# Optimization experiments

Measured on AMD Instinct MI355X. Metric: run time of the kernel, lower is better.

## Reference

```python
import jax, jax.numpy as jnp
import numpy as np
from jax import lax

B_, L, DM = 2, 2048, 1024
DI, N, K, R = 2048, 16, 4, 64  # d_inner, d_state, d_conv, dt_rank
EPS = 1e-5


def setup_inputs() -> dict:
    key = jax.random.key(0)
    ks = jax.random.split(key, 12)
    w = lambda k, s: (jax.random.normal(k, s, dtype=jnp.float32) * 0.02)
    inp = {
        "x": jax.random.normal(ks[0], (B_, L, DM), dtype=jnp.float32),
        "hormone_vectors": jax.random.normal(ks[1], (B_, 64), dtype=jnp.float32),
        "norm_w": jnp.ones((DM,), dtype=jnp.float32),
        "in_proj_w": w(ks[2], (DM, 2 * DI)),
        "conv_w": w(ks[3], (DI, K)),
        "conv_b": jnp.zeros((DI,), dtype=jnp.float32),
        "x_proj_w": w(ks[4], (DI, R + 2 * N)),
        "dt_proj_w": w(ks[5], (R, DI)),
        "dt_proj_b": jax.random.uniform(ks[6], (DI,), dtype=jnp.float32, minval=-4.0, maxval=-2.0),
        "A_log": jnp.log(jnp.broadcast_to(jnp.arange(1, N + 1, dtype=jnp.float32), (DI, N))),
        "D": jnp.ones((DI,), dtype=jnp.float32),
        "out_proj_w": w(ks[7], (DI, DM)),
    }
    return inp


def _rmsnorm(x, w, eps=EPS):
    var = jnp.mean(x * x, axis=-1, keepdims=True)
    return x * lax.rsqrt(var + eps) * w


def _causal_depthwise_conv(u, conv_w, conv_b):
    # u: [B,L,DI] -> causal depthwise conv along L with kernel K
    lhs = jnp.transpose(u, (0, 2, 1))  # [B,DI,L]
    lhs = jnp.pad(lhs, ((0, 0), (0, 0), (K - 1, 0)))
    rhs = conv_w[:, None, :]  # [DI,1,K]
    out = lax.conv_general_dilated(
        lhs, rhs, window_strides=(1,), padding="VALID",
        dimension_numbers=("NCH", "OIH", "NCH"), feature_group_count=DI)
    return jnp.transpose(out, (0, 2, 1)) + conv_b  # [B,L,DI]


def _mamba_mixer(h, in_proj_w, conv_w, conv_b, x_proj_w, dt_proj_w, dt_proj_b,
                 A_log, D, out_proj_w):
    xz = h @ in_proj_w                       # [B,L,2*DI]
    u, z = jnp.split(xz, 2, axis=-1)         # each [B,L,DI]
    u = jax.nn.silu(_causal_depthwise_conv(u, conv_w, conv_b))

    xdbl = u @ x_proj_w                      # [B,L,R+2N]
    dt_r = xdbl[..., :R]
    Bm = xdbl[..., R:R + N]                  # [B,L,N]
    Cm = xdbl[..., R + N:]                   # [B,L,N]
    dt = jax.nn.softplus(dt_r @ dt_proj_w + dt_proj_b)  # [B,L,DI]
    A = -jnp.exp(A_log)                      # [DI,N]

    def step(hst, inp):
        dt_t, B_t, C_t, u_t = inp            # [B,DI],[B,N],[B,N],[B,DI]
        dA = jnp.exp(dt_t[..., None] * A)                         # [B,DI,N]
        dBu = dt_t[..., None] * B_t[:, None, :] * u_t[..., None]  # [B,DI,N]
        hst = dA * hst + dBu
        y = jnp.einsum("bdn,bn->bd", hst, C_t)
        return hst, y

    xs = (jnp.swapaxes(dt, 0, 1), jnp.swapaxes(Bm, 0, 1),
          jnp.swapaxes(Cm, 0, 1), jnp.swapaxes(u, 0, 1))
    h0 = jnp.zeros((u.shape[0], DI, N), dtype=u.dtype)
    _, ys = lax.scan(step, h0, xs)
    y = jnp.swapaxes(ys, 0, 1) + u * D       # [B,L,DI]
    y = y * jax.nn.silu(z)
    return y @ out_proj_w                    # [B,L,DM]


def reference(x, hormone_vectors, norm_w, in_proj_w, conv_w, conv_b, x_proj_w,
              dt_proj_w, dt_proj_b, A_log, D, out_proj_w):
    del hormone_vectors  # unused, matching original module
    h = _rmsnorm(x, norm_w)
    return x + _mamba_mixer(h, in_proj_w, conv_w, conv_b, x_proj_w,
                            dt_proj_w, dt_proj_b, A_log, D, out_proj_w)
```

## Files before the change

kernel.cpp:

```cpp
#include <hip/hip_runtime.h>
#include <stddef.h>

#define B_SZ 2
#define L_SZ 2048
#define DM_SZ 1024
#define DI_SZ 2048
#define N_SZ 16
#define K_SZ 4
#define R_SZ 64
#define ROWS (B_SZ * L_SZ)
#define CH 32
#define NCH (L_SZ / CH)
#define PS_SLICE (B_SZ * DI_SZ * N_SZ)

typedef unsigned short u16;
typedef unsigned int u32;
typedef short bf16x8 __attribute__((ext_vector_type(8)));
typedef float f32x4 __attribute__((ext_vector_type(4)));

__device__ __forceinline__ u16 f2bf(float f) {
    union { float f; u32 i; } v; v.f = f;
    u32 x = v.i;
    return (u16)((x + 0x7FFFu + ((x >> 16) & 1u)) >> 16);
}
__device__ __forceinline__ float bf2f(u16 u) {
    union { u32 i; float f; } v; v.i = ((u32)u) << 16; return v.f;
}

__device__ __forceinline__ void gload_lds16(const void* g, void* l) {
    __builtin_amdgcn_global_load_lds((const __attribute__((address_space(1))) u32*)g,
                                     (__attribute__((address_space(3))) u32*)l, 16, 0, 0);
}

__global__ __launch_bounds__(256) void rmsnorm_kernel(const float* __restrict__ x,
                                                      const float* __restrict__ w,
                                                      u16* __restrict__ h) {
    const int row = blockIdx.x;
    const float* xr = x + (size_t)row * DM_SZ;
    const int t4 = threadIdx.x * 4;
    float4 xv = *(const float4*)(xr + t4);
    float ss = xv.x * xv.x + xv.y * xv.y + xv.z * xv.z + xv.w * xv.w;
    #pragma unroll
    for (int off = 32; off; off >>= 1) ss += __shfl_down(ss, off);
    __shared__ float red[4];
    if ((threadIdx.x & 63) == 0) red[threadIdx.x >> 6] = ss;
    __syncthreads();
    float tot = red[0] + red[1] + red[2] + red[3];
    float rs = rsqrtf(tot * (1.0f / DM_SZ) + 1e-5f);
    float4 wv = *(const float4*)(w + t4);
    ushort4 o;
    o.x = f2bf(xv.x * rs * wv.x);
    o.y = f2bf(xv.y * rs * wv.y);
    o.z = f2bf(xv.z * rs * wv.z);
    o.w = f2bf(xv.w * rs * wv.w);
    *(ushort4*)(h + (size_t)row * DM_SZ + t4) = o;
}

__global__ __launch_bounds__(256) void transpose_bf16_kernel(const float* __restrict__ W,
                                                             u16* __restrict__ Wt,
                                                             int K, int N) {
    __shared__ float t[32][33];
    const int n0 = blockIdx.x * 32, k0 = blockIdx.y * 32;
    const int tx = threadIdx.x & 31, ty = threadIdx.x >> 5;
    #pragma unroll
    for (int p = 0; p < 4; ++p)
        t[ty + p * 8][tx] = W[(size_t)(k0 + ty + p * 8) * N + n0 + tx];
    __syncthreads();
    #pragma unroll
    for (int p = 0; p < 4; ++p)
        Wt[(size_t)(n0 + ty + p * 8) * K + k0 + tx] = f2bf(t[tx][ty + p * 8]);
}

template <bool HAS_RESID>
__global__ __launch_bounds__(256, 2) void mfma_gemm_bt(const u16* __restrict__ A,
                                                       const u16* __restrict__ Bt,
                                                       float* __restrict__ C,
                                                       const float* __restrict__ resid,
                                                       int M, int N, int Kd) {
    __shared__ __align__(16) u16 As[128 * 32];
    __shared__ __align__(16) u16 Bs[128 * 32];
    const int tid = threadIdx.x;
    const int lane = tid & 63;
    const int w = tid >> 6;
    const int wm = w >> 1, wn = w & 1;
    const int bm = blockIdx.y * 128, bn = blockIdx.x * 128;

    const int r0 = (w * 2 + 0) * 16 + (lane >> 2);
    const int r1 = (w * 2 + 1) * 16 + (lane >> 2);
    const int kc = (lane & 3) * 8;
    const u16* Aq0 = A + (size_t)(bm + r0) * Kd + kc;
    const u16* Aq1 = A + (size_t)(bm + r1) * Kd + kc;
    const u16* Bq0 = Bt + (size_t)(bn + r0) * Kd + kc;
    const u16* Bq1 = Bt + (size_t)(bn + r1) * Kd + kc;
    u16* lA0 = As + (w * 2 + 0) * 512;
    u16* lA1 = As + (w * 2 + 1) * 512;
    u16* lB0 = Bs + (w * 2 + 0) * 512;
    u16* lB1 = Bs + (w * 2 + 1) * 512;

    f32x4 acc[4][4] = {};
    const int fm = (lane & 15);
    const int q8 = (lane >> 4) * 8;

    for (int k0 = 0; k0 < Kd; k0 += 32) {
        gload_lds16(Aq0 + k0, lA0);
        gload_lds16(Aq1 + k0, lA1);
        gload_lds16(Bq0 + k0, lB0);
        gload_lds16(Bq1 + k0, lB1);
        __syncthreads();
        bf16x8 af[4], bf[4];
        #pragma unroll
        for (int i = 0; i < 4; ++i)
            af[i] = *(const bf16x8*)&As[(wm * 64 + i * 16 + fm) * 32 + q8];
        #pragma unroll
        for (int j = 0; j < 4; ++j)
            bf[j] = *(const bf16x8*)&Bs[(wn * 64 + j * 16 + fm) * 32 + q8];
        #pragma unroll
        for (int i = 0; i < 4; ++i)
            #pragma unroll
            for (int j = 0; j < 4; ++j)
                acc[i][j] = __builtin_amdgcn_mfma_f32_16x16x32_bf16(af[i], bf[j], acc[i][j], 0, 0, 0);
        __syncthreads();
    }

    const int crow0 = bm + wm * 64 + (lane >> 4) * 4;
    const int ccol0 = bn + wn * 64 + (lane & 15);
    #pragma unroll
    for (int i = 0; i < 4; ++i) {
        #pragma unroll
        for (int r = 0; r < 4; ++r) {
            const int row = crow0 + i * 16 + r;
            #pragma unroll
            for (int j = 0; j < 4; ++j) {
                const int col = ccol0 + j * 16;
                float v = acc[i][j][r];
                if (HAS_RESID) v += resid[(size_t)row * N + col];
                C[(size_t)row * N + col] = v;
            }
        }
    }
}

__global__ __launch_bounds__(256) void conv_silu_kernel(const float* __restrict__ xz,
                                                        const float* __restrict__ cw,
                                                        const float* __restrict__ cb,
                                                        u16* __restrict__ u) {
    const int idx = blockIdx.x * 256 + threadIdx.x;
    const int d = idx & (DI_SZ - 1);
    const int r = idx >> 11;
    const int t = r & (L_SZ - 1);
    float4 w4 = *(const float4*)(cw + (d << 2));
    const float w[4] = {w4.x, w4.y, w4.z, w4.w};
    float acc = cb[d];
    const float* base = xz + (size_t)r * (2 * DI_SZ) + d;
    #pragma unroll
    for (int k = 0; k < 4; ++k) {
        int tt = t - 3 + k;
        if (tt >= 0) acc += base[(ptrdiff_t)(k - 3) * (2 * DI_SZ)] * w[k];
    }
    u[idx] = f2bf(acc / (1.0f + __expf(-acc)));
}

__global__ __launch_bounds__(256) void xproj_mfma(const u16* __restrict__ ubf,
                                                  const u16* __restrict__ Wt,
                                                  float* __restrict__ xdbl) {
    const int lane = threadIdx.x & 63;
    const int w = threadIdx.x >> 6;
    const int m0 = blockIdx.x * 64 + w * 16;
    const int k0 = blockIdx.y * 256;
    const int fr = lane & 15;
    const int q8 = (lane >> 4) * 8;
    const u16* Arow = ubf + (size_t)(m0 + fr) * DI_SZ + k0 + q8;
    const u16* Brow = Wt + (size_t)fr * DI_SZ + k0 + q8;
    f32x4 acc[6] = {};
    #pragma unroll 2
    for (int kk = 0; kk < 256; kk += 32) {
        bf16x8 a = *(const bf16x8*)(Arow + kk);
        #pragma unroll
        for (int j = 0; j < 6; ++j) {
            bf16x8 b = *(const bf16x8*)(Brow + (size_t)(j * 16) * DI_SZ + kk);
            acc[j] = __builtin_amdgcn_mfma_f32_16x16x32_bf16(a, b, acc[j], 0, 0, 0);
        }
    }
    const int row0 = m0 + (lane >> 4) * 4;
    const int col = lane & 15;
    #pragma unroll
    for (int j = 0; j < 6; ++j)
        #pragma unroll
        for (int r = 0; r < 4; ++r)
            atomicAdd(&xdbl[(size_t)(row0 + r) * 96 + j * 16 + col], acc[j][r]);
}

__global__ __launch_bounds__(256) void dtslice_bf16_kernel(const float* __restrict__ xdbl,
                                                           u16* __restrict__ out) {
    const int idx = blockIdx.x * 256 + threadIdx.x;
    const int r = idx >> 6, k = idx & 63;
    out[idx] = f2bf(xdbl[(size_t)r * 96 + k]);
}

__global__ __launch_bounds__(256, 2) void dtproj_mfma(const u16* __restrict__ Axd,
                                                      const u16* __restrict__ Wt,
                                                      const float* __restrict__ bias,
                                                      u16* __restrict__ dt) {
    __shared__ __align__(16) u16 As[128 * 64];
    __shared__ __align__(16) u16 Bs[128 * 64];
    const int tid = threadIdx.x;
    const int lane = tid & 63;
    const int w = tid >> 6;
    const int wm = w >> 1, wn = w & 1;
    const int bm = blockIdx.y * 128, bn = blockIdx.x * 128;

    #pragma unroll
    for (int q = 0; q < 4; ++q) {
        const int rr = (w * 4 + q) * 8 + (lane >> 3);
        const int kc = (lane & 7) * 8;
        gload_lds16(Axd + (size_t)(bm + rr) * 64 + kc, As + (w * 4 + q) * 512);
        gload_lds16(Wt  + (size_t)(bn + rr) * 64 + kc, Bs + (w * 4 + q) * 512);
    }
    __syncthreads();

    const int fm = lane & 15;
    const int q8 = (lane >> 4) * 8;
    f32x4 acc[4][4] = {};
    #pragma unroll
    for (int k0 = 0; k0 < 64; k0 += 32) {
        bf16x8 af[4], bf[4];
        #pragma unroll
        for (int i = 0; i < 4; ++i)
            af[i] = *(const bf16x8*)&As[(wm * 64 + i * 16 + fm) * 64 + k0 + q8];
        #pragma unroll
        for (int j = 0; j < 4; ++j)
            bf[j] = *(const bf16x8*)&Bs[(wn * 64 + j * 16 + fm) * 64 + k0 + q8];
        #pragma unroll
        for (int i = 0; i < 4; ++i)
            #pragma unroll
            for (int j = 0; j < 4; ++j)
                acc[i][j] = __builtin_amdgcn_mfma_f32_16x16x32_bf16(af[i], bf[j], acc[i][j], 0, 0, 0);
    }

    const int crow0 = bm + wm * 64 + (lane >> 4) * 4;
    const int ccol0 = bn + wn * 64 + (lane & 15);
    #pragma unroll
    for (int j = 0; j < 4; ++j) {
        const int col = ccol0 + j * 16;
        const float b = bias[col];
        #pragma unroll
        for (int i = 0; i < 4; ++i) {
            #pragma unroll
            for (int r = 0; r < 4; ++r) {
                const int row = crow0 + i * 16 + r;
                float v = acc[i][j][r] + b;
                float sp = (v > 20.0f) ? v : log1pf(__expf(v));
                dt[(size_t)row * DI_SZ + col] = f2bf(sp);
            }
        }
    }
}

__global__ __launch_bounds__(64) void scan_pass1(const u16* __restrict__ dt,
                                                 const u16* __restrict__ u,
                                                 const float* __restrict__ xdbl,
                                                 const float* __restrict__ A_log,
                                                 float* __restrict__ P,
                                                 float* __restrict__ S) {
    const int c     = blockIdx.x & (NCH - 1);
    const int dtile = (blockIdx.x >> 6) & 31;
    const int b     = blockIdx.x >> 11;
    const int d     = dtile * 64 + threadIdx.x;
    float A[N_SZ];
    #pragma unroll
    for (int n = 0; n < N_SZ; ++n) A[n] = -expf(A_log[d * N_SZ + n]);
    __shared__ __align__(16) float bs[CH][16];
    const size_t rbase = (size_t)b * L_SZ + c * CH;
    for (int idx = threadIdx.x; idx < CH * 16; idx += 64) {
        int tt = idx >> 4, j = idx & 15;
        bs[tt][j] = xdbl[(rbase + tt) * 96 + 64 + j];
    }
    __syncthreads();
    float h[N_SZ] = {};
    float p[N_SZ];
    #pragma unroll
    for (int n = 0; n < N_SZ; ++n) p[n] = 1.0f;
    float dtv = bf2f(dt[rbase * DI_SZ + d]);
    float uv  = bf2f(u[rbase * DI_SZ + d]);
    for (int ti = 0; ti < CH; ++ti) {
        float dtn = 0.0f, un = 0.0f;
        if (ti + 1 < CH) {
            dtn = bf2f(dt[(rbase + ti + 1) * DI_SZ + d]);
            un  = bf2f(u[(rbase + ti + 1) * DI_SZ + d]);
        }
        const float dtu = dtv * uv;
        float bv[N_SZ];
        #pragma unroll
        for (int q = 0; q < 4; ++q) *(float4*)&bv[q * 4] = *(const float4*)&bs[ti][q * 4];
        #pragma unroll
        for (int n = 0; n < N_SZ; ++n) {
            float dA = __expf(dtv * A[n]);
            p[n] *= dA;
            h[n] = dA * h[n] + dtu * bv[n];
        }
        dtv = dtn; uv = un;
    }
    const size_t base = (size_t)c * PS_SLICE + ((size_t)b * DI_SZ + d) * N_SZ;
    #pragma unroll
    for (int q = 0; q < 4; ++q) {
        *(float4*)&P[base + q * 4] = make_float4(p[q*4], p[q*4+1], p[q*4+2], p[q*4+3]);
        *(float4*)&S[base + q * 4] = make_float4(h[q*4], h[q*4+1], h[q*4+2], h[q*4+3]);
    }
}

__global__ __launch_bounds__(256) void scan_pass2(float* __restrict__ P,
                                                  float* __restrict__ S) {
    const int i = blockIdx.x * 256 + threadIdx.x;
    float h = 0.0f;
    for (int c = 0; c < NCH; ++c) {
        const size_t idx = (size_t)c * PS_SLICE + i;
        const float p = P[idx];
        const float s = S[idx];
        S[idx] = h;
        h = p * h + s;
    }
}

__global__ __launch_bounds__(64) void scan_pass3(const u16* __restrict__ dt,
                                                 const u16* __restrict__ u,
                                                 const float* __restrict__ xz,
                                                 const float* __restrict__ xdbl,
                                                 const float* __restrict__ A_log,
                                                 const float* __restrict__ Dw,
                                                 const float* __restrict__ H0,
                                                 u16* __restrict__ y) {
    const int c     = blockIdx.x & (NCH - 1);
    const int dtile = (blockIdx.x >> 6) & 31;
    const int b     = blockIdx.x >> 11;
    const int d     = dtile * 64 + threadIdx.x;
    float A[N_SZ];
    #pragma unroll
    for (int n = 0; n < N_SZ; ++n) A[n] = -expf(A_log[d * N_SZ + n]);
    const float Dd = Dw[d];
    __shared__ __align__(16) float bc[CH][32];
    const size_t rbase = (size_t)b * L_SZ + c * CH;
    for (int idx = threadIdx.x; idx < CH * 32; idx += 64) {
        int tt = idx >> 5, j = idx & 31;
        bc[tt][j] = xdbl[(rbase + tt) * 96 + 64 + j];
    }
    __syncthreads();
    float h[N_SZ];
    const size_t hbase = (size_t)c * PS_SLICE + ((size_t)b * DI_SZ + d) * N_SZ;
    #pragma unroll
    for (int q = 0; q < 4; ++q) *(float4*)&h[q * 4] = *(const float4*)&H0[hbase + q * 4];
    float dtv = bf2f(dt[rbase * DI_SZ + d]);
    float uv  = bf2f(u[rbase * DI_SZ + d]);
    float zv  = xz[rbase * (2 * DI_SZ) + DI_SZ + d];
    for (int ti = 0; ti < CH; ++ti) {
        float dtn = 0.0f, un = 0.0f, zn = 0.0f;
        if (ti + 1 < CH) {
            const size_t rn = rbase + ti + 1;
            dtn = bf2f(dt[rn * DI_SZ + d]);
            un  = bf2f(u[rn * DI_SZ + d]);
            zn  = xz[rn * (2 * DI_SZ) + DI_SZ + d];
        }
        const float dtu = dtv * uv;
        float bv[32];
        #pragma unroll
        for (int q = 0; q < 8; ++q) *(float4*)&bv[q * 4] = *(const float4*)&bc[ti][q * 4];
        float yv = 0.0f;
        #pragma unroll
        for (int n = 0; n < N_SZ; ++n) {
            float dA = __expf(dtv * A[n]);
            h[n] = dA * h[n] + dtu * bv[n];
            yv += h[n] * bv[16 + n];
        }
        const float sz = zv / (1.0f + __expf(-zv));
        y[(rbase + ti) * DI_SZ + d] = f2bf((yv + uv * Dd) * sz);
        dtv = dtn; uv = un; zv = zn;
    }
}

extern "C" void kernel_launch(void* const* d_in, const int* in_sizes, int n_in,
                              void* d_out, int out_size, void* d_ws, size_t ws_size,
                              hipStream_t stream) {
    const float* x         = (const float*)d_in[0];
    const float* norm_w    = (const float*)d_in[2];
    const float* in_proj_w = (const float*)d_in[3];
    const float* conv_w    = (const float*)d_in[4];
    const float* conv_b    = (const float*)d_in[5];
    const float* x_proj_w  = (const float*)d_in[6];
    const float* dt_proj_w = (const float*)d_in[7];
    const float* dt_proj_b = (const float*)d_in[8];
    const float* A_log     = (const float*)d_in[9];
    const float* Dw        = (const float*)d_in[10];
    const float* out_proj_w= (const float*)d_in[11];
    float* out = (float*)d_out;

    char* ws = (char*)d_ws;
    size_t off = 0;
    u16* y      = (u16*)(ws + off);    off += (size_t)ROWS * DI_SZ * 2;
    u16* h      = y;
    float* xz   = (float*)(ws + off);  off += (size_t)ROWS * 2 * DI_SZ * 4;
    u16* u      = (u16*)(ws + off);    off += (size_t)ROWS * DI_SZ * 2;
    float* xdbl = (float*)(ws + off);  off += (size_t)ROWS * 96 * 4;
    u16* dt     = (u16*)(ws + off);    off += (size_t)ROWS * DI_SZ * 2;
    float* P    = (float*)(ws + off);  off += (size_t)NCH * PS_SLICE * 4;
    float* S    = (float*)(ws + off);  off += (size_t)NCH * PS_SLICE * 4;
    u16* ipw_t  = (u16*)(ws + off);    off += (size_t)(2 * DI_SZ) * DM_SZ * 2;
    u16* opw_t  = (u16*)(ws + off);    off += (size_t)DM_SZ * DI_SZ * 2;
    u16* xpw_t  = (u16*)(ws + off);    off += (size_t)96 * DI_SZ * 2;
    u16* dtw_t  = (u16*)(ws + off);    off += (size_t)DI_SZ * R_SZ * 2;
    u16* xdbl_bf= (u16*)(ws + off);    off += (size_t)ROWS * R_SZ * 2;
    (void)ws_size; (void)out_size; (void)n_in; (void)in_sizes;

    rmsnorm_kernel<<<ROWS, 256, 0, stream>>>(x, norm_w, h);
    transpose_bf16_kernel<<<dim3(2 * DI_SZ / 32, DM_SZ / 32), 256, 0, stream>>>(
        in_proj_w, ipw_t, DM_SZ, 2 * DI_SZ);
    transpose_bf16_kernel<<<dim3(DM_SZ / 32, DI_SZ / 32), 256, 0, stream>>>(
        out_proj_w, opw_t, DI_SZ, DM_SZ);
    transpose_bf16_kernel<<<dim3(96 / 32, DI_SZ / 32), 256, 0, stream>>>(
        x_proj_w, xpw_t, DI_SZ, 96);
    transpose_bf16_kernel<<<dim3(DI_SZ / 32, R_SZ / 32), 256, 0, stream>>>(
        dt_proj_w, dtw_t, R_SZ, DI_SZ);
    mfma_gemm_bt<false><<<dim3(2 * DI_SZ / 128, ROWS / 128), 256, 0, stream>>>(
        h, ipw_t, xz, nullptr, ROWS, 2 * DI_SZ, DM_SZ);
    conv_silu_kernel<<<(ROWS * DI_SZ) / 256, 256, 0, stream>>>(xz, conv_w, conv_b, u);
    hipMemsetAsync(xdbl, 0, (size_t)ROWS * 96 * 4, stream);
    xproj_mfma<<<dim3(ROWS / 64, 8), 256, 0, stream>>>(u, xpw_t, xdbl);
    dtslice_bf16_kernel<<<(ROWS * R_SZ) / 256, 256, 0, stream>>>(xdbl, xdbl_bf);
    dtproj_mfma<<<dim3(DI_SZ / 128, ROWS / 128), 256, 0, stream>>>(
        xdbl_bf, dtw_t, dt_proj_b, dt);
    scan_pass1<<<B_SZ * 32 * NCH, 64, 0, stream>>>(dt, u, xdbl, A_log, P, S);
    scan_pass2<<<PS_SLICE / 256, 256, 0, stream>>>(P, S);
    scan_pass3<<<B_SZ * 32 * NCH, 64, 0, stream>>>(dt, u, xz, xdbl, A_log, Dw, S, y);
    mfma_gemm_bt<true><<<dim3(DM_SZ / 128, ROWS / 128), 256, 0, stream>>>(
        y, opw_t, out, x, ROWS, DM_SZ, DI_SZ);
}
```

Baseline: 375.1 us.

## Store xz in bf16, merge weight transposes, retile out-proj, widen scan chunks

Several changes at once. The in-projection output xz is now stored as bf16 instead of fp32, which halves its write and read traffic in the conv and scan stages. The four weight-transpose launches are merged into one kernel, and the conv/silu kernel is vectorised to four channels per thread. The out-projection GEMM uses 128x64 tiles so more blocks fill the CUs, and the scan chunk length doubles from 32 to 64, giving fewer chunks and a smaller prefix pass. The cost is lower precision for the gate z and the conv input, and less parallelism in the scan.

```diff
diff --git a/kernel.cpp b/kernel.cpp
--- a/kernel.cpp
+++ b/kernel.cpp
@@ -9,7 +9,7 @@
 #define K_SZ 4
 #define R_SZ 64
 #define ROWS (B_SZ * L_SZ)
-#define CH 32
+#define CH 64
 #define NCH (L_SZ / CH)
 #define PS_SLICE (B_SZ * DI_SZ * N_SZ)
 
@@ -56,11 +56,11 @@
     *(ushort4*)(h + (size_t)row * DM_SZ + t4) = o;
 }
 
-__global__ __launch_bounds__(256) void transpose_bf16_kernel(const float* __restrict__ W,
-                                                             u16* __restrict__ Wt,
-                                                             int K, int N) {
+__device__ __forceinline__ void transpose_tile(const float* __restrict__ W,
+                                               u16* __restrict__ Wt,
+                                               int K, int N, int bx, int by) {
     __shared__ float t[32][33];
-    const int n0 = blockIdx.x * 32, k0 = blockIdx.y * 32;
+    const int n0 = bx * 32, k0 = by * 32;
     const int tx = threadIdx.x & 31, ty = threadIdx.x >> 5;
     #pragma unroll
     for (int p = 0; p < 4; ++p)
@@ -71,11 +71,28 @@
         Wt[(size_t)(n0 + ty + p * 8) * K + k0 + tx] = f2bf(t[tx][ty + p * 8]);
 }
 
-template <bool HAS_RESID>
-__global__ __launch_bounds__(256, 2) void mfma_gemm_bt(const u16* __restrict__ A,
+__global__ __launch_bounds__(256) void transpose_all(const float* __restrict__ ipw, u16* __restrict__ ipw_t,
+                                                     const float* __restrict__ opw, u16* __restrict__ opw_t,
+                                                     const float* __restrict__ xpw, u16* __restrict__ xpw_t,
+                                                     const float* __restrict__ dtw, u16* __restrict__ dtw_t) {
+    int b = blockIdx.x;
+    if (b < 4096) {
+        transpose_tile(ipw, ipw_t, DM_SZ, 2 * DI_SZ, b & 127, b >> 7);
+    } else if (b < 6144) {
+        b -= 4096;
+        transpose_tile(opw, opw_t, DI_SZ, DM_SZ, b & 31, b >> 5);
+    } else if (b < 6336) {
+        b -= 6144;
+        transpose_tile(xpw, xpw_t, DI_SZ, 96, b % 3, b / 3);
+    } else {
+        b -= 6336;
+        transpose_tile(dtw, dtw_t, R_SZ, DI_SZ, b & 63, b >> 6);
+    }
+}
+
+__global__ __launch_bounds__(256, 2) void mfma_gemm_xz(const u16* __restrict__ A,
                                                        const u16* __restrict__ Bt,
-                                                       float* __restrict__ C,
-                                                       const float* __restrict__ resid,
+                                                       u16* __restrict__ C,
                                                        int M, int N, int Kd) {
     __shared__ __align__(16) u16 As[128 * 32];
     __shared__ __align__(16) u16 Bs[128 * 32];
@@ -125,39 +142,111 @@
     const int crow0 = bm + wm * 64 + (lane >> 4) * 4;
     const int ccol0 = bn + wn * 64 + (lane & 15);
     #pragma unroll
-    for (int i = 0; i < 4; ++i) {
+    for (int i = 0; i < 4; ++i)
         #pragma unroll
         for (int r = 0; r < 4; ++r) {
             const int row = crow0 + i * 16 + r;
             #pragma unroll
-            for (int j = 0; j < 4; ++j) {
+            for (int j = 0; j < 4; ++j)
+                C[(size_t)row * N + ccol0 + j * 16] = f2bf(acc[i][j][r]);
+        }
+}
+
+__global__ __launch_bounds__(256, 2) void mfma_gemm_rn(const u16* __restrict__ A,
+                                                       const u16* __restrict__ Bt,
+                                                       float* __restrict__ C,
+                                                       const float* __restrict__ resid,
+                                                       int M, int N, int Kd) {
+    __shared__ __align__(16) u16 As[128 * 32];
+    __shared__ __align__(16) u16 Bs[64 * 32];
+    const int tid = threadIdx.x;
+    const int lane = tid & 63;
+    const int w = tid >> 6;
+    const int wm = w >> 1, wn = w & 1;
+    const int bm = blockIdx.y * 128, bn = blockIdx.x * 64;
+
+    const int rA0 = (w * 2 + 0) * 16 + (lane >> 2);
+    const int rA1 = (w * 2 + 1) * 16 + (lane >> 2);
+    const int rB  = w * 16 + (lane >> 2);
+    const int kc = (lane & 3) * 8;
+    const u16* Aq0 = A + (size_t)(bm + rA0) * Kd + kc;
+    const u16* Aq1 = A + (size_t)(bm + rA1) * Kd + kc;
+    const u16* Bq  = Bt + (size_t)(bn + rB) * Kd + kc;
+    u16* lA0 = As + (w * 2 + 0) * 512;
+    u16* lA1 = As + (w * 2 + 1) * 512;
+    u16* lB  = Bs + w * 512;
+
+    f32x4 acc[4][2] = {};
+    const int fm = (lane & 15);
+    const int q8 = (lane >> 4) * 8;
+
+    for (int k0 = 0; k0 < Kd; k0 += 32) {
+        gload_lds16(Aq0 + k0, lA0);
+        gload_lds16(Aq1 + k0, lA1);
+        gload_lds16(Bq + k0, lB);
+        __syncthreads();
+        bf16x8 af[4], bf[2];
+        #pragma unroll
+        for (int i = 0; i < 4; ++i)
+            af[i] = *(const bf16x8*)&As[(wm * 64 + i * 16 + fm) * 32 + q8];
+        #pragma unroll
+        for (int j = 0; j < 2; ++j)
+            bf[j] = *(const bf16x8*)&Bs[(wn * 32 + j * 16 + fm) * 32 + q8];
+        #pragma unroll
+        for (int i = 0; i < 4; ++i)
+            #pragma unroll
+            for (int j = 0; j < 2; ++j)
+                acc[i][j] = __builtin_amdgcn_mfma_f32_16x16x32_bf16(af[i], bf[j], acc[i][j], 0, 0, 0);
+        __syncthreads();
+    }
+
+    const int crow0 = bm + wm * 64 + (lane >> 4) * 4;
+    const int ccol0 = bn + wn * 32 + (lane & 15);
+    #pragma unroll
+    for (int i = 0; i < 4; ++i)
+        #pragma unroll
+        for (int r = 0; r < 4; ++r) {
+            const int row = crow0 + i * 16 + r;
+            #pragma unroll
+            for (int j = 0; j < 2; ++j) {
                 const int col = ccol0 + j * 16;
-                float v = acc[i][j][r];
-                if (HAS_RESID) v += resid[(size_t)row * N + col];
-                C[(size_t)row * N + col] = v;
+                C[(size_t)row * N + col] = acc[i][j][r] + resid[(size_t)row * N + col];
             }
         }
-    }
-}
-
-__global__ __launch_bounds__(256) void conv_silu_kernel(const float* __restrict__ xz,
+}
+
+__global__ __launch_bounds__(256) void conv_silu_kernel(const u16* __restrict__ xz,
                                                         const float* __restrict__ cw,
                                                         const float* __restrict__ cb,
                                                         u16* __restrict__ u) {
-    const int idx = blockIdx.x * 256 + threadIdx.x;
-    const int d = idx & (DI_SZ - 1);
-    const int r = idx >> 11;
+    const int idx4 = blockIdx.x * 256 + threadIdx.x;
+    const int d4 = (idx4 & (DI_SZ / 4 - 1)) * 4;
+    const int r = idx4 >> 9;
     const int t = r & (L_SZ - 1);
-    float4 w4 = *(const float4*)(cw + (d << 2));
-    const float w[4] = {w4.x, w4.y, w4.z, w4.w};
-    float acc = cb[d];
-    const float* base = xz + (size_t)r * (2 * DI_SZ) + d;
+    float acc[4];
+    float4 cbv = *(const float4*)(cb + d4);
+    acc[0] = cbv.x; acc[1] = cbv.y; acc[2] = cbv.z; acc[3] = cbv.w;
+    float wv[4][4];
+    #pragma unroll
+    for (int j = 0; j < 4; ++j) *(float4*)wv[j] = *(const float4*)(cw + (d4 + j) * 4);
+    const u16* base = xz + (size_t)r * (2 * DI_SZ) + d4;
     #pragma unroll
     for (int k = 0; k < 4; ++k) {
         int tt = t - 3 + k;
-        if (tt >= 0) acc += base[(ptrdiff_t)(k - 3) * (2 * DI_SZ)] * w[k];
-    }
-    u[idx] = f2bf(acc / (1.0f + __expf(-acc)));
+        if (tt >= 0) {
+            ushort4 xv = *(const ushort4*)(base + (ptrdiff_t)(k - 3) * (2 * DI_SZ));
+            acc[0] += bf2f(xv.x) * wv[0][k];
+            acc[1] += bf2f(xv.y) * wv[1][k];
+            acc[2] += bf2f(xv.z) * wv[2][k];
+            acc[3] += bf2f(xv.w) * wv[3][k];
+        }
+    }
+    ushort4 o;
+    o.x = f2bf(acc[0] / (1.0f + __expf(-acc[0])));
+    o.y = f2bf(acc[1] / (1.0f + __expf(-acc[1])));
+    o.z = f2bf(acc[2] / (1.0f + __expf(-acc[2])));
+    o.w = f2bf(acc[3] / (1.0f + __expf(-acc[3])));
+    *(ushort4*)(u + (size_t)r * DI_SZ + d4) = o;
 }
 
 __global__ __launch_bounds__(256) void xproj_mfma(const u16* __restrict__ ubf,
@@ -244,7 +333,7 @@
         const int col = ccol0 + j * 16;
         const float b = bias[col];
         #pragma unroll
-        for (int i = 0; i < 4; ++i) {
+        for (int i = 0; i < 4; ++i)
             #pragma unroll
             for (int r = 0; r < 4; ++r) {
                 const int row = crow0 + i * 16 + r;
@@ -252,7 +341,6 @@
                 float sp = (v > 20.0f) ? v : log1pf(__expf(v));
                 dt[(size_t)row * DI_SZ + col] = f2bf(sp);
             }
-        }
     }
 }
 
@@ -263,8 +351,8 @@
                                                  float* __restrict__ P,
                                                  float* __restrict__ S) {
     const int c     = blockIdx.x & (NCH - 1);
-    const int dtile = (blockIdx.x >> 6) & 31;
-    const int b     = blockIdx.x >> 11;
+    const int dtile = (blockIdx.x >> 5) & 31;
+    const int b     = blockIdx.x >> 10;
     const int d     = dtile * 64 + threadIdx.x;
     float A[N_SZ];
     #pragma unroll
@@ -323,15 +411,15 @@
 
 __global__ __launch_bounds__(64) void scan_pass3(const u16* __restrict__ dt,
                                                  const u16* __restrict__ u,
-                                                 const float* __restrict__ xz,
+                                                 const u16* __restrict__ xz,
                                                  const float* __restrict__ xdbl,
                                                  const float* __restrict__ A_log,
                                                  const float* __restrict__ Dw,
                                                  const float* __restrict__ H0,
                                                  u16* __restrict__ y) {
     const int c     = blockIdx.x & (NCH - 1);
-    const int dtile = (blockIdx.x >> 6) & 31;
-    const int b     = blockIdx.x >> 11;
+    const int dtile = (blockIdx.x >> 5) & 31;
+    const int b     = blockIdx.x >> 10;
     const int d     = dtile * 64 + threadIdx.x;
     float A[N_SZ];
     #pragma unroll
@@ -350,14 +438,14 @@
     for (int q = 0; q < 4; ++q) *(float4*)&h[q * 4] = *(const float4*)&H0[hbase + q * 4];
     float dtv = bf2f(dt[rbase * DI_SZ + d]);
     float uv  = bf2f(u[rbase * DI_SZ + d]);
-    float zv  = xz[rbase * (2 * DI_SZ) + DI_SZ + d];
+    float zv  = bf2f(xz[rbase * (2 * DI_SZ) + DI_SZ + d]);
     for (int ti = 0; ti < CH; ++ti) {
         float dtn = 0.0f, un = 0.0f, zn = 0.0f;
         if (ti + 1 < CH) {
             const size_t rn = rbase + ti + 1;
             dtn = bf2f(dt[rn * DI_SZ + d]);
             un  = bf2f(u[rn * DI_SZ + d]);
-            zn  = xz[rn * (2 * DI_SZ) + DI_SZ + d];
+            zn  = bf2f(xz[rn * (2 * DI_SZ) + DI_SZ + d]);
         }
         const float dtu = dtv * uv;
         float bv[32];
@@ -396,7 +484,7 @@
     size_t off = 0;
     u16* y      = (u16*)(ws + off);    off += (size_t)ROWS * DI_SZ * 2;
     u16* h      = y;
-    float* xz   = (float*)(ws + off);  off += (size_t)ROWS * 2 * DI_SZ * 4;
+    u16* xz     = (u16*)(ws + off);    off += (size_t)ROWS * 2 * DI_SZ * 2;
     u16* u      = (u16*)(ws + off);    off += (size_t)ROWS * DI_SZ * 2;
     float* xdbl = (float*)(ws + off);  off += (size_t)ROWS * 96 * 4;
     u16* dt     = (u16*)(ws + off);    off += (size_t)ROWS * DI_SZ * 2;
@@ -410,17 +498,11 @@
     (void)ws_size; (void)out_size; (void)n_in; (void)in_sizes;
 
     rmsnorm_kernel<<<ROWS, 256, 0, stream>>>(x, norm_w, h);
-    transpose_bf16_kernel<<<dim3(2 * DI_SZ / 32, DM_SZ / 32), 256, 0, stream>>>(
-        in_proj_w, ipw_t, DM_SZ, 2 * DI_SZ);
-    transpose_bf16_kernel<<<dim3(DM_SZ / 32, DI_SZ / 32), 256, 0, stream>>>(
-        out_proj_w, opw_t, DI_SZ, DM_SZ);
-    transpose_bf16_kernel<<<dim3(96 / 32, DI_SZ / 32), 256, 0, stream>>>(
-        x_proj_w, xpw_t, DI_SZ, 96);
-    transpose_bf16_kernel<<<dim3(DI_SZ / 32, R_SZ / 32), 256, 0, stream>>>(
-        dt_proj_w, dtw_t, R_SZ, DI_SZ);
-    mfma_gemm_bt<false><<<dim3(2 * DI_SZ / 128, ROWS / 128), 256, 0, stream>>>(
-        h, ipw_t, xz, nullptr, ROWS, 2 * DI_SZ, DM_SZ);
-    conv_silu_kernel<<<(ROWS * DI_SZ) / 256, 256, 0, stream>>>(xz, conv_w, conv_b, u);
+    transpose_all<<<6464, 256, 0, stream>>>(in_proj_w, ipw_t, out_proj_w, opw_t,
+                                            x_proj_w, xpw_t, dt_proj_w, dtw_t);
+    mfma_gemm_xz<<<dim3(2 * DI_SZ / 128, ROWS / 128), 256, 0, stream>>>(
+        h, ipw_t, xz, ROWS, 2 * DI_SZ, DM_SZ);
+    conv_silu_kernel<<<(ROWS * DI_SZ / 4) / 256, 256, 0, stream>>>(xz, conv_w, conv_b, u);
     hipMemsetAsync(xdbl, 0, (size_t)ROWS * 96 * 4, stream);
     xproj_mfma<<<dim3(ROWS / 64, 8), 256, 0, stream>>>(u, xpw_t, xdbl);
     dtslice_bf16_kernel<<<(ROWS * R_SZ) / 256, 256, 0, stream>>>(xdbl, xdbl_bf);
@@ -429,6 +511,6 @@
     scan_pass1<<<B_SZ * 32 * NCH, 64, 0, stream>>>(dt, u, xdbl, A_log, P, S);
     scan_pass2<<<PS_SLICE / 256, 256, 0, stream>>>(P, S);
     scan_pass3<<<B_SZ * 32 * NCH, 64, 0, stream>>>(dt, u, xz, xdbl, A_log, Dw, S, y);
-    mfma_gemm_bt<true><<<dim3(DM_SZ / 128, ROWS / 128), 256, 0, stream>>>(
+    mfma_gemm_rn<<<dim3(DM_SZ / 64, ROWS / 128), 256, 0, stream>>>(
         y, opw_t, out, x, ROWS, DM_SZ, DI_SZ);
 }
```

New measurement: 364.4 us. 2.8% less time.
